# Kernel optimization log

Measured on AMD Instinct MI355X. Metric: run time of the kernel, lower is better.

## Reference

```python
import jax, jax.numpy as jnp
import numpy as np

B, H, W, C = 2, 256, 256, 96
NH, WS, SS = 3, 8, 4
HD = C // NH
N = WS * WS              # tokens per window
NWIMG = (H // WS) * (W // WS)  # windows per image
MLP = 4 * C
EPS = 1e-5

def _np_attn_mask():
    img = np.zeros((H, W))
    sl = (slice(0, -WS), slice(-WS, -SS), slice(-SS, None))
    cnt = 0
    for a in sl:
        for b in sl:
            img[a, b] = cnt
            cnt += 1
    m = img.reshape(H // WS, WS, W // WS, WS).transpose(0, 2, 1, 3).reshape(-1, N)
    am = m[:, None, :] - m[:, :, None]
    return np.where(am != 0, -100.0, 0.0).astype(np.float32)

def _np_rel_index():
    coords = np.stack(np.meshgrid(np.arange(WS), np.arange(WS), indexing='ij'))
    cf = coords.reshape(2, -1)
    rel = (cf[:, :, None] - cf[:, None, :]).transpose(1, 2, 0).copy()
    rel[..., 0] += WS - 1
    rel[..., 1] += WS - 1
    rel[..., 0] *= 2 * WS - 1
    return rel.sum(-1)

def _np_coords_table():
    r = np.arange(-(WS - 1), WS, dtype=np.float32)
    t = np.stack(np.meshgrid(r, r, indexing='ij'), axis=-1) / (WS - 1) * 8.0
    t = np.sign(t) * np.log2(np.abs(t) + 1.0) / np.log2(8.0)
    return t.reshape(-1, 2)

ATTN_MASK = jnp.asarray(_np_attn_mask())          # [NWIMG, N, N]
REL_INDEX = jnp.asarray(_np_rel_index().reshape(-1))
COORDS_TABLE = jnp.asarray(_np_coords_table())    # [(2WS-1)^2, 2]

def setup_inputs():
    key = jax.random.key(0)
    ks = jax.random.split(key, 16)
    s = 0.02
    return {
        'hidden_states': jax.random.normal(ks[0], (B, H * W, C), jnp.float32),
        'time': jax.random.uniform(ks[1], (B,), jnp.float32),
        'q_w': jax.random.normal(ks[2], (C, C), jnp.float32) * s,
        'q_b': jnp.zeros((C,), jnp.float32),
        'k_w': jax.random.normal(ks[3], (C, C), jnp.float32) * s,
        'v_w': jax.random.normal(ks[4], (C, C), jnp.float32) * s,
        'v_b': jnp.zeros((C,), jnp.float32),
        'proj_w': jax.random.normal(ks[5], (C, C), jnp.float32) * s,
        'proj_b': jnp.zeros((C,), jnp.float32),
        'logit_scale': jnp.full((NH, 1, 1), jnp.log(10.0), jnp.float32),
        'cpb_w1': jax.random.normal(ks[6], (2, 512), jnp.float32) * s,
        'cpb_b1': jnp.zeros((512,), jnp.float32),
        'cpb_w2': jax.random.normal(ks[7], (512, NH), jnp.float32) * s,
        'lnb_ww': jax.random.normal(ks[8], (1, C), jnp.float32) * s,
        'lnb_wb': jnp.ones((C,), jnp.float32),
        'lnb_bw': jax.random.normal(ks[9], (1, C), jnp.float32) * s,
        'lnb_bb': jnp.zeros((C,), jnp.float32),
        'lna_ww': jax.random.normal(ks[10], (1, C), jnp.float32) * s,
        'lna_wb': jnp.ones((C,), jnp.float32),
        'lna_bw': jax.random.normal(ks[11], (1, C), jnp.float32) * s,
        'lna_bb': jnp.zeros((C,), jnp.float32),
        'fc1_w': jax.random.normal(ks[12], (C, MLP), jnp.float32) * s,
        'fc1_b': jnp.zeros((MLP,), jnp.float32),
        'fc2_w': jax.random.normal(ks[13], (MLP, C), jnp.float32) * s,
        'fc2_b': jnp.zeros((C,), jnp.float32),
    }

def _cln(x, time, ww, wb, bw, bb):
    # ConditionalLayerNorm: stats over channels, affine params from time via Linear(1, C)
    mean = x.mean(-1, keepdims=True)
    var = (x * x).mean(-1, keepdims=True) - mean * mean
    xn = (x - mean) / jnp.sqrt(var + EPS)
    t = time.reshape(-1, 1)
    w = (t @ ww + wb)[:, None, :]
    b = (t @ bw + bb)[:, None, :]
    return w * xn + b

def reference(hidden_states, time, q_w, q_b, k_w, v_w, v_b, proj_w, proj_b, logit_scale, cpb_w1, cpb_b1, cpb_w2, lnb_ww, lnb_wb, lnb_bw, lnb_bb, lna_ww, lna_wb, lna_bw, lna_bb, fc1_w, fc1_b, fc2_w, fc2_b):
    shortcut = hidden_states
    x = hidden_states.reshape(B, H, W, C)
    x = jnp.roll(x, (-SS, -SS), axis=(1, 2))  # cyclic shift
    # window partition -> [nW, N, C]
    xw = x.reshape(B, H // WS, WS, W // WS, WS, C).transpose(0, 1, 3, 2, 4, 5).reshape(-1, N, C)
    nW = B * NWIMG
    q = (xw @ q_w + q_b).reshape(nW, N, NH, HD).transpose(0, 2, 1, 3)
    k = (xw @ k_w).reshape(nW, N, NH, HD).transpose(0, 2, 1, 3)  # key has no bias in Swinv2
    v = (xw @ v_w + v_b).reshape(nW, N, NH, HD).transpose(0, 2, 1, 3)
    # cosine attention with clamped learnable log temperature
    qn = q / jnp.maximum(jnp.linalg.norm(q, axis=-1, keepdims=True), 1e-12)
    kn = k / jnp.maximum(jnp.linalg.norm(k, axis=-1, keepdims=True), 1e-12)
    scale = jnp.exp(jnp.minimum(logit_scale, jnp.log(100.0)))  # [NH,1,1]
    attn = jnp.einsum('whnd,whmd->whnm', qn, kn) * scale[None]
    # continuous relative position bias: MLP(2->512->NH) over log-spaced coords
    bias_table = jax.nn.relu(COORDS_TABLE @ cpb_w1 + cpb_b1) @ cpb_w2
    bias = bias_table[REL_INDEX].reshape(N, N, NH).transpose(2, 0, 1)
    attn = attn + 16.0 * jax.nn.sigmoid(bias)[None]
    # shifted-window mask
    attn = attn.reshape(B, NWIMG, NH, N, N) + ATTN_MASK[None, :, None]
    attn = jax.nn.softmax(attn.reshape(nW, NH, N, N), axis=-1)
    ctx = jnp.einsum('whnm,whmd->whnd', attn, v).transpose(0, 2, 1, 3).reshape(nW, N, C)
    ctx = ctx @ proj_w + proj_b
    # window reverse + un-shift
    xr = ctx.reshape(B, H // WS, W // WS, WS, WS, C).transpose(0, 1, 3, 2, 4, 5).reshape(B, H, W, C)
    xr = jnp.roll(xr, (SS, SS), axis=(1, 2))
    attn_out = xr.reshape(B, H * W, C)
    # post-norm residual (Swin v2 style) with conditional LN
    hs = shortcut + _cln(attn_out, time, lnb_ww, lnb_wb, lnb_bw, lnb_bb)
    inter = jax.nn.gelu(hs @ fc1_w + fc1_b, approximate=False)
    mlp_out = inter @ fc2_w + fc2_b
    return hs + _cln(mlp_out, time, lna_ww, lna_wb, lna_bw, lna_bb)
```

## Files before the change

### kernel.cpp

```cpp
#include <hip/hip_runtime.h>
#include <hip/hip_bf16.h>

typedef __bf16 bf16_t;
typedef bf16_t bf16x8 __attribute__((ext_vector_type(8)));
typedef bf16_t bf16x4 __attribute__((ext_vector_type(4)));
typedef float  f32x4  __attribute__((ext_vector_type(4)));

#define LDC 104
#define LDT 72
#define LDP 70
#define LDG 392

#define WS_WQ    0
#define WS_WK    19968
#define WS_WV    39936
#define WS_WP    59904
#define WS_FC1   79872
#define WS_FC2   159744
#define WS_BIAS  235008

__device__ __forceinline__ f32x4 mfma16(bf16x8 a, bf16x8 b, f32x4 c) {
    return __builtin_amdgcn_mfma_f32_16x16x32_bf16(a, b, c, 0, 0, 0);
}

__device__ __forceinline__ float cpbf(int v) {
    float x = (float)v * (8.0f / 7.0f);
    float l = log2f(fabsf(x) + 1.0f) * (1.0f / 3.0f);
    return x < 0.f ? -l : l;
}

__device__ __forceinline__ int regcnt(int t, int hw, int ww) {
    int r = t >> 3, c = t & 7;
    int rr = (hw == 31) ? (r < 4 ? 1 : 2) : 0;
    int cc = (ww == 31) ? (c < 4 ? 1 : 2) : 0;
    return rr * 3 + cc;
}

__global__ __launch_bounds__(512) void k0_prep(
    const float* __restrict__ qw, const float* __restrict__ kw,
    const float* __restrict__ vw, const float* __restrict__ pw,
    const float* __restrict__ fc1w, const float* __restrict__ fc2w,
    const float* __restrict__ cw1, const float* __restrict__ cb1,
    const float* __restrict__ cw2, char* __restrict__ ws)
{
    int tid = threadIdx.x;
    if (blockIdx.x == 0) {
        __shared__ float part[450 * 3];
        __shared__ float table[225 * 3];
        if (tid < 450) {
            int pos = tid >> 1, half = tid & 1;
            int ia = pos / 15, ib = pos % 15;
            float c0 = cpbf(ia - 7), c1 = cpbf(ib - 7);
            float a0 = 0.f, a1 = 0.f, a2 = 0.f;
            int j0 = half * 256;
            for (int j = j0; j < j0 + 256; ++j) {
                float h = fmaf(c0, cw1[j], fmaf(c1, cw1[512 + j], cb1[j]));
                h = fmaxf(h, 0.f);
                a0 = fmaf(h, cw2[j * 3 + 0], a0);
                a1 = fmaf(h, cw2[j * 3 + 1], a1);
                a2 = fmaf(h, cw2[j * 3 + 2], a2);
            }
            part[tid * 3 + 0] = a0; part[tid * 3 + 1] = a1; part[tid * 3 + 2] = a2;
        }
        __syncthreads();
        if (tid < 225) {
            table[tid * 3 + 0] = part[(2 * tid) * 3 + 0] + part[(2 * tid + 1) * 3 + 0];
            table[tid * 3 + 1] = part[(2 * tid) * 3 + 1] + part[(2 * tid + 1) * 3 + 1];
            table[tid * 3 + 2] = part[(2 * tid) * 3 + 2] + part[(2 * tid + 1) * 3 + 2];
        }
        __syncthreads();
        float* bias = (float*)(ws + WS_BIAS);
        for (int e = tid; e < 3 * 64 * 64; e += 512) {
            int h = e >> 12, nm = e & 4095, n = nm >> 6, m = nm & 63;
            int dr = (n >> 3) - (m >> 3) + 7, dc = (n & 7) - (m & 7) + 7;
            float t = table[(dr * 15 + dc) * 3 + h];
            bias[e] = 16.f / (1.f + __expf(-t));
        }
    } else {
        int rid = (blockIdx.x - 1) * 512 + tid;
        if (rid < 9216) {
            int which = rid / 2304, r = rid % 2304;
            int i = r / 24, o4 = r % 24;
            const float* src = which == 0 ? qw : which == 1 ? kw : which == 2 ? vw : pw;
            float4 u = *(const float4*)(src + i * 96 + 4 * o4);
            bf16_t* dst = (bf16_t*)(ws + WS_WQ + which * 19968);
            dst[(4 * o4 + 0) * LDC + i] = (bf16_t)u.x;
            dst[(4 * o4 + 1) * LDC + i] = (bf16_t)u.y;
            dst[(4 * o4 + 2) * LDC + i] = (bf16_t)u.z;
            dst[(4 * o4 + 3) * LDC + i] = (bf16_t)u.w;
        } else if (rid < 18432) {
            int r = rid - 9216;
            int i = r / 96, m4 = r % 96;
            float4 u = *(const float4*)(fc1w + i * 384 + 4 * m4);
            bf16_t* dst = (bf16_t*)(ws + WS_FC1);
            dst[(4 * m4 + 0) * LDC + i] = (bf16_t)u.x;
            dst[(4 * m4 + 1) * LDC + i] = (bf16_t)u.y;
            dst[(4 * m4 + 2) * LDC + i] = (bf16_t)u.z;
            dst[(4 * m4 + 3) * LDC + i] = (bf16_t)u.w;
        } else {
            int r = rid - 18432;
            int g = r / 24, o4 = r % 24;
            float4 u = *(const float4*)(fc2w + g * 96 + 4 * o4);
            bf16_t* dst = (bf16_t*)(ws + WS_FC2);
            dst[(4 * o4 + 0) * LDG + g] = (bf16_t)u.x;
            dst[(4 * o4 + 1) * LDG + g] = (bf16_t)u.y;
            dst[(4 * o4 + 2) * LDG + g] = (bf16_t)u.z;
            dst[(4 * o4 + 3) * LDG + g] = (bf16_t)u.w;
        }
    }
}

__global__ __launch_bounds__(256, 4) void kA_attn(
    const float* __restrict__ hidden, const float* __restrict__ tv,
    const float* __restrict__ qb, const float* __restrict__ vb,
    const float* __restrict__ pb, const float* __restrict__ lsc,
    const float* __restrict__ lnww, const float* __restrict__ lnwb,
    const float* __restrict__ lnbw, const float* __restrict__ lnbb,
    const char* __restrict__ ws, float* __restrict__ hs)
{
    __shared__ __align__(16) char sm[40704];
    bf16_t* vT   = (bf16_t*)(sm + 0);
    bf16_t* qn   = (bf16_t*)(sm + 13824);
    bf16_t* kn   = (bf16_t*)(sm + 27136);
    bf16_t* P    = (bf16_t*)(sm + 13824);
    bf16_t* ctxb = (bf16_t*)(sm + 0);

    const int tid = threadIdx.x;
    const int wv = tid >> 6, lane = tid & 63, lg = lane >> 4, lr = lane & 15;
    const int wid = blockIdx.x;
    const int bat = wid >> 10, wim = wid & 1023, hw = wim >> 5, wwi = wim & 31;

    {
        bf16x8 af[3];
        {
            int tok = 16 * wv + lr;
            int gr = ((hw << 3) + (tok >> 3) + 4) & 255;
            int gc = ((wwi << 3) + (tok & 7) + 4) & 255;
            const float* xb = hidden + (((size_t)bat << 16) + (gr << 8) + gc) * 96;
            #pragma unroll
            for (int ks = 0; ks < 3; ++ks) {
                float4 u0 = *(const float4*)(xb + 32 * ks + 8 * lg);
                float4 u1 = *(const float4*)(xb + 32 * ks + 8 * lg + 4);
                bf16x8 f;
                f[0] = (bf16_t)u0.x; f[1] = (bf16_t)u0.y; f[2] = (bf16_t)u0.z; f[3] = (bf16_t)u0.w;
                f[4] = (bf16_t)u1.x; f[5] = (bf16_t)u1.y; f[6] = (bf16_t)u1.z; f[7] = (bf16_t)u1.w;
                af[ks] = f;
            }
        }
        const bf16_t* Wq = (const bf16_t*)(ws + WS_WQ);
        const bf16_t* Wk = (const bf16_t*)(ws + WS_WK);
        const bf16_t* Wv = (const bf16_t*)(ws + WS_WV);

        #pragma unroll
        for (int h = 0; h < 3; ++h) {
            f32x4 a0 = {0.f,0.f,0.f,0.f}, a1 = {0.f,0.f,0.f,0.f};
            #pragma unroll
            for (int ks = 0; ks < 3; ++ks) {
                a0 = mfma16(af[ks], *(const bf16x8*)(Wq + (32 * h + lr) * LDC + 32 * ks + 8 * lg), a0);
                a1 = mfma16(af[ks], *(const bf16x8*)(Wq + (32 * h + 16 + lr) * LDC + 32 * ks + 8 * lg), a1);
            }
            float b0 = qb[32 * h + lr], b1 = qb[32 * h + 16 + lr];
            #pragma unroll
            for (int j = 0; j < 4; ++j) { a0[j] += b0; a1[j] += b1; }
            #pragma unroll
            for (int j = 0; j < 4; ++j) {
                float s = a0[j] * a0[j] + a1[j] * a1[j];
                s += __shfl_xor(s, 1); s += __shfl_xor(s, 2); s += __shfl_xor(s, 4); s += __shfl_xor(s, 8);
                float inv = 1.f / fmaxf(sqrtf(s), 1e-12f);
                int row = 16 * wv + 4 * lg + j;
                qn[row * LDC + 32 * h + lr]      = (bf16_t)(a0[j] * inv);
                qn[row * LDC + 32 * h + 16 + lr] = (bf16_t)(a1[j] * inv);
            }
        }
        #pragma unroll
        for (int h = 0; h < 3; ++h) {
            f32x4 a0 = {0.f,0.f,0.f,0.f}, a1 = {0.f,0.f,0.f,0.f};
            #pragma unroll
            for (int ks = 0; ks < 3; ++ks) {
                a0 = mfma16(af[ks], *(const bf16x8*)(Wk + (32 * h + lr) * LDC + 32 * ks + 8 * lg), a0);
                a1 = mfma16(af[ks], *(const bf16x8*)(Wk + (32 * h + 16 + lr) * LDC + 32 * ks + 8 * lg), a1);
            }
            #pragma unroll
            for (int j = 0; j < 4; ++j) {
                float s = a0[j] * a0[j] + a1[j] * a1[j];
                s += __shfl_xor(s, 1); s += __shfl_xor(s, 2); s += __shfl_xor(s, 4); s += __shfl_xor(s, 8);
                float inv = 1.f / fmaxf(sqrtf(s), 1e-12f);
                int row = 16 * wv + 4 * lg + j;
                kn[row * LDC + 32 * h + lr]      = (bf16_t)(a0[j] * inv);
                kn[row * LDC + 32 * h + 16 + lr] = (bf16_t)(a1[j] * inv);
            }
        }
        #pragma unroll
        for (int nt = 0; nt < 6; ++nt) {
            f32x4 a = {0.f,0.f,0.f,0.f};
            #pragma unroll
            for (int ks = 0; ks < 3; ++ks)
                a = mfma16(af[ks], *(const bf16x8*)(Wv + (16 * nt + lr) * LDC + 32 * ks + 8 * lg), a);
            float bv_ = vb[16 * nt + lr];
            bf16x4 pk;
            #pragma unroll
            for (int j = 0; j < 4; ++j) pk[j] = (bf16_t)(a[j] + bv_);
            *(bf16x4*)(vT + (16 * nt + lr) * LDT + 16 * wv + 4 * lg) = pk;
        }
    }
    __syncthreads();

    {
        f32x4 s[3][4];
        #pragma unroll
        for (int h = 0; h < 3; ++h) {
            bf16x8 aq = *(const bf16x8*)(qn + (16 * wv + lr) * LDC + 32 * h + 8 * lg);
            bf16x8 bk[4];
            #pragma unroll
            for (int f = 0; f < 4; ++f)
                bk[f] = *(const bf16x8*)(kn + (16 * f + lr) * LDC + 32 * h + 8 * lg);
            #pragma unroll
            for (int f = 0; f < 4; ++f) {
                f32x4 z = {0.f,0.f,0.f,0.f};
                s[h][f] = mfma16(aq, bk[f], z);
            }
        }
        __syncthreads();

        float ls[3];
        #pragma unroll
        for (int h = 0; h < 3; ++h) ls[h] = __expf(fminf(lsc[h], 4.6051702f));
        const float* biasT = (const float*)(ws + WS_BIAS);
        int cntm[4], cnti[4];
        #pragma unroll
        for (int f = 0; f < 4; ++f) cntm[f] = regcnt(16 * f + lr, hw, wwi);
        #pragma unroll
        for (int j = 0; j < 4; ++j) cnti[j] = regcnt(16 * wv + 4 * lg + j, hw, wwi);
        #pragma unroll
        for (int h = 0; h < 3; ++h) {
            #pragma unroll
            for (int f = 0; f < 4; ++f)
                #pragma unroll
                for (int j = 0; j < 4; ++j) {
                    float b = biasT[(h << 12) + (16 * wv + 4 * lg + j) * 64 + 16 * f + lr];
                    float mk = (cnti[j] != cntm[f]) ? -100.f : 0.f;
                    s[h][f][j] = fmaf(s[h][f][j], ls[h], b + mk);
                }
            #pragma unroll
            for (int j = 0; j < 4; ++j) {
                float mx = fmaxf(fmaxf(s[h][0][j], s[h][1][j]), fmaxf(s[h][2][j], s[h][3][j]));
                mx = fmaxf(mx, __shfl_xor(mx, 1)); mx = fmaxf(mx, __shfl_xor(mx, 2));
                mx = fmaxf(mx, __shfl_xor(mx, 4)); mx = fmaxf(mx, __shfl_xor(mx, 8));
                float sum = 0.f;
                #pragma unroll
                for (int f = 0; f < 4; ++f) { float e = __expf(s[h][f][j] - mx); s[h][f][j] = e; sum += e; }
                sum += __shfl_xor(sum, 1); sum += __shfl_xor(sum, 2); sum += __shfl_xor(sum, 4); sum += __shfl_xor(sum, 8);
                float inv = 1.f / sum;
                int row = 16 * wv + 4 * lg + j;
                #pragma unroll
                for (int f = 0; f < 4; ++f)
                    P[h * 64 * LDP + row * LDP + 16 * f + lr] = (bf16_t)(s[h][f][j] * inv);
            }
        }
    }
    __syncthreads();

    {
        f32x4 ctx[6];
        #pragma unroll
        for (int t = 0; t < 6; ++t) { f32x4 z = {0.f,0.f,0.f,0.f}; ctx[t] = z; }
        #pragma unroll
        for (int h = 0; h < 3; ++h) {
            bf16x8 ap[2], bv2[2][2];
            #pragma unroll
            for (int ks = 0; ks < 2; ++ks) {
                ap[ks] = *(const bf16x8*)(P + h * 64 * LDP + (16 * wv + lr) * LDP + 32 * ks + 8 * lg);
                #pragma unroll
                for (int dt = 0; dt < 2; ++dt)
                    bv2[dt][ks] = *(const bf16x8*)(vT + (32 * h + 16 * dt + lr) * LDT + 32 * ks + 8 * lg);
            }
            #pragma unroll
            for (int ks = 0; ks < 2; ++ks)
                #pragma unroll
                for (int dt = 0; dt < 2; ++dt)
                    ctx[2 * h + dt] = mfma16(ap[ks], bv2[dt][ks], ctx[2 * h + dt]);
        }
        __syncthreads();
        #pragma unroll
        for (int t = 0; t < 6; ++t)
            #pragma unroll
            for (int j = 0; j < 4; ++j)
                ctxb[(16 * wv + 4 * lg + j) * LDC + 16 * t + lr] = (bf16_t)ctx[t][j];
    }
    __syncthreads();

    {
        const bf16_t* Wp = (const bf16_t*)(ws + WS_WP);
        bf16x8 af[3];
        #pragma unroll
        for (int ks = 0; ks < 3; ++ks) af[ks] = *(const bf16x8*)(ctxb + (16 * wv + lr) * LDC + 32 * ks + 8 * lg);
        f32x4 acc[6];
        #pragma unroll
        for (int nt = 0; nt < 6; ++nt) {
            f32x4 a = {0.f,0.f,0.f,0.f};
            #pragma unroll
            for (int ks = 0; ks < 3; ++ks)
                a = mfma16(af[ks], *(const bf16x8*)(Wp + (16 * nt + lr) * LDC + 32 * ks + 8 * lg), a);
            float bp = pb[16 * nt + lr];
            #pragma unroll
            for (int j = 0; j < 4; ++j) a[j] += bp;
            acc[nt] = a;
        }
        float tb = tv[bat];
        #pragma unroll
        for (int j = 0; j < 4; ++j) {
            float smn = 0.f, sq = 0.f;
            #pragma unroll
            for (int t = 0; t < 6; ++t) { float v = acc[t][j]; smn += v; sq = fmaf(v, v, sq); }
            smn += __shfl_xor(smn, 1); smn += __shfl_xor(smn, 2); smn += __shfl_xor(smn, 4); smn += __shfl_xor(smn, 8);
            sq  += __shfl_xor(sq, 1);  sq  += __shfl_xor(sq, 2);  sq  += __shfl_xor(sq, 4);  sq  += __shfl_xor(sq, 8);
            float mean = smn * (1.f / 96.f);
            float var  = sq * (1.f / 96.f) - mean * mean;
            float rstd = rsqrtf(var + 1e-5f);
            int trow = 16 * wv + 4 * lg + j;
            int gr = ((hw << 3) + (trow >> 3) + 4) & 255;
            int gc = ((wwi << 3) + (trow & 7) + 4) & 255;
            size_t gbase = (((size_t)bat << 16) + (gr << 8) + gc) * 96;
            #pragma unroll
            for (int t = 0; t < 6; ++t) {
                int col = 16 * t + lr;
                float w = fmaf(tb, lnww[col], lnwb[col]);
                float b = fmaf(tb, lnbw[col], lnbb[col]);
                float xn = (acc[t][j] - mean) * rstd;
                hs[gbase + col] = hidden[gbase + col] + fmaf(w, xn, b);
            }
        }
    }
}

__global__ __launch_bounds__(256, 3) void kB_mlp(
    const float* __restrict__ tv, const float* __restrict__ fc1b,
    const float* __restrict__ fc2b,
    const float* __restrict__ lnww, const float* __restrict__ lnwb,
    const float* __restrict__ lnbw, const float* __restrict__ lnbb,
    const char* __restrict__ ws, float* __restrict__ io)
{
    __shared__ __align__(16) bf16_t gbuf[64 * LDG];

    const int tid = threadIdx.x;
    const int wv = tid >> 6, lane = tid & 63, lg = lane >> 4, lr = lane & 15;
    const size_t t0 = (size_t)blockIdx.x * 64;

    bf16x8 hf[3];
    #pragma unroll
    for (int ks = 0; ks < 3; ++ks) {
        const float* p = io + (t0 + 16 * wv + lr) * 96 + 32 * ks + 8 * lg;
        float4 u0 = *(const float4*)p;
        float4 u1 = *(const float4*)(p + 4);
        bf16x8 f;
        f[0] = (bf16_t)u0.x; f[1] = (bf16_t)u0.y; f[2] = (bf16_t)u0.z; f[3] = (bf16_t)u0.w;
        f[4] = (bf16_t)u1.x; f[5] = (bf16_t)u1.y; f[6] = (bf16_t)u1.z; f[7] = (bf16_t)u1.w;
        hf[ks] = f;
    }

    const bf16_t* w1 = (const bf16_t*)(ws + WS_FC1);
    const bf16_t* w2 = (const bf16_t*)(ws + WS_FC2);

    #pragma unroll 6
    for (int nt = 0; nt < 24; ++nt) {
        f32x4 a = {0.f,0.f,0.f,0.f};
        #pragma unroll
        for (int ks = 0; ks < 3; ++ks)
            a = mfma16(hf[ks], *(const bf16x8*)(w1 + (16 * nt + lr) * LDC + 32 * ks + 8 * lg), a);
        float bb = fc1b[16 * nt + lr];
        #pragma unroll
        for (int j = 0; j < 4; ++j) {
            float x = a[j] + bb;
            float u = 0.7978845608f * fmaf(0.044715f * x, x * x, x);
            float t = __expf(2.f * u);
            float g = x - x * __builtin_amdgcn_rcpf(t + 1.f);
            gbuf[(16 * wv + 4 * lg + j) * LDG + 16 * nt + lr] = (bf16_t)g;
        }
    }
    __syncthreads();

    f32x4 mlp[6];
    #pragma unroll
    for (int t = 0; t < 6; ++t) { f32x4 z = {0.f,0.f,0.f,0.f}; mlp[t] = z; }
    #pragma unroll
    for (int kk = 0; kk < 12; ++kk) {
        bf16x8 gf = *(const bf16x8*)(gbuf + (16 * wv + lr) * LDG + 32 * kk + 8 * lg);
        #pragma unroll
        for (int nt = 0; nt < 6; ++nt)
            mlp[nt] = mfma16(gf, *(const bf16x8*)(w2 + (16 * nt + lr) * LDG + 32 * kk + 8 * lg), mlp[nt]);
    }

    float tb = tv[t0 >> 16];
    #pragma unroll
    for (int nt = 0; nt < 6; ++nt) {
        float bb = fc2b[16 * nt + lr];
        #pragma unroll
        for (int j = 0; j < 4; ++j) mlp[nt][j] += bb;
    }
    #pragma unroll
    for (int j = 0; j < 4; ++j) {
        float smn = 0.f, sq = 0.f;
        #pragma unroll
        for (int t = 0; t < 6; ++t) { float v = mlp[t][j]; smn += v; sq = fmaf(v, v, sq); }
        smn += __shfl_xor(smn, 1); smn += __shfl_xor(smn, 2); smn += __shfl_xor(smn, 4); smn += __shfl_xor(smn, 8);
        sq  += __shfl_xor(sq, 1);  sq  += __shfl_xor(sq, 2);  sq  += __shfl_xor(sq, 4);  sq  += __shfl_xor(sq, 8);
        float mean = smn * (1.f / 96.f);
        float var  = sq * (1.f / 96.f) - mean * mean;
        float rstd = rsqrtf(var + 1e-5f);
        size_t row = t0 + 16 * wv + 4 * lg + j;
        #pragma unroll
        for (int t = 0; t < 6; ++t) {
            int col = 16 * t + lr;
            float w = fmaf(tb, lnww[col], lnwb[col]);
            float b = fmaf(tb, lnbw[col], lnbb[col]);
            float xn = (mlp[t][j] - mean) * rstd;
            io[row * 96 + col] = io[row * 96 + col] + fmaf(w, xn, b);
        }
    }
}

extern "C" void kernel_launch(void* const* d_in, const int* in_sizes, int n_in,
                              void* d_out, int out_size, void* d_ws, size_t ws_size,
                              hipStream_t stream)
{
    const float* hidden = (const float*)d_in[0];
    const float* tv     = (const float*)d_in[1];
    const float* q_w    = (const float*)d_in[2];
    const float* q_b    = (const float*)d_in[3];
    const float* k_w    = (const float*)d_in[4];
    const float* v_w    = (const float*)d_in[5];
    const float* v_b    = (const float*)d_in[6];
    const float* p_w    = (const float*)d_in[7];
    const float* p_b    = (const float*)d_in[8];
    const float* lsc    = (const float*)d_in[9];
    const float* cw1    = (const float*)d_in[10];
    const float* cb1    = (const float*)d_in[11];
    const float* cw2    = (const float*)d_in[12];
    const float* lnb_ww = (const float*)d_in[13];
    const float* lnb_wb = (const float*)d_in[14];
    const float* lnb_bw = (const float*)d_in[15];
    const float* lnb_bb = (const float*)d_in[16];
    const float* lna_ww = (const float*)d_in[17];
    const float* lna_wb = (const float*)d_in[18];
    const float* lna_bw = (const float*)d_in[19];
    const float* lna_bb = (const float*)d_in[20];
    const float* fc1_w  = (const float*)d_in[21];
    const float* fc1_b  = (const float*)d_in[22];
    const float* fc2_w  = (const float*)d_in[23];
    const float* fc2_b  = (const float*)d_in[24];
    char* ws = (char*)d_ws;
    float* out = (float*)d_out;

    k0_prep<<<dim3(55), dim3(512), 0, stream>>>(q_w, k_w, v_w, p_w, fc1_w, fc2_w, cw1, cb1, cw2, ws);
    kA_attn<<<dim3(2048), dim3(256), 0, stream>>>(hidden, tv, q_b, v_b, p_b, lsc,
                                                  lnb_ww, lnb_wb, lnb_bw, lnb_bb, ws, out);
    kB_mlp<<<dim3(2048), dim3(256), 0, stream>>>(tv, fc1_b, fc2_b,
                                                 lna_ww, lna_wb, lna_bw, lna_bb, ws, out);
}
```

Baseline: 332.1 us.

## Parallelize CPB table prep and batch weight/bias loads ahead of MFMA chains

```diff
diff --git a/kernel.cpp b/kernel.cpp
--- a/kernel.cpp
+++ b/kernel.cpp
@@ -18,6 +18,7 @@
 #define WS_FC1   79872
 #define WS_FC2   159744
 #define WS_BIAS  235008
+#define WS_TBL   284160
 
 __device__ __forceinline__ f32x4 mfma16(bf16x8 a, bf16x8 b, f32x4 c) {
     return __builtin_amdgcn_mfma_f32_16x16x32_bf16(a, b, c, 0, 0, 0);
@@ -36,48 +37,46 @@
     return rr * 3 + cc;
 }
 
-__global__ __launch_bounds__(512) void k0_prep(
+__global__ __launch_bounds__(256) void k0a_cpb(
+    const float* __restrict__ cw1, const float* __restrict__ cb1,
+    const float* __restrict__ cw2, char* __restrict__ ws)
+{
+    const int wv = threadIdx.x >> 6, lane = threadIdx.x & 63;
+    const int e = blockIdx.x * 4 + wv;
+    if (e >= 225) return;
+    int ia = e / 15, ib = e % 15;
+    float c0 = cpbf(ia - 7), c1 = cpbf(ib - 7);
+    float a0 = 0.f, a1 = 0.f, a2 = 0.f;
+    #pragma unroll
+    for (int c = 0; c < 8; ++c) {
+        int j = c * 64 + lane;
+        float h = fmaf(c0, cw1[j], fmaf(c1, cw1[512 + j], cb1[j]));
+        h = fmaxf(h, 0.f);
+        a0 = fmaf(h, cw2[j * 3 + 0], a0);
+        a1 = fmaf(h, cw2[j * 3 + 1], a1);
+        a2 = fmaf(h, cw2[j * 3 + 2], a2);
+    }
+    #pragma unroll
+    for (int m = 1; m < 64; m <<= 1) {
+        a0 += __shfl_xor(a0, m);
+        a1 += __shfl_xor(a1, m);
+        a2 += __shfl_xor(a2, m);
+    }
+    if (lane == 0) {
+        float* tbl = (float*)(ws + WS_TBL);
+        tbl[e * 3 + 0] = a0; tbl[e * 3 + 1] = a1; tbl[e * 3 + 2] = a2;
+    }
+}
+
+__global__ __launch_bounds__(512) void k0w_prep(
     const float* __restrict__ qw, const float* __restrict__ kw,
     const float* __restrict__ vw, const float* __restrict__ pw,
     const float* __restrict__ fc1w, const float* __restrict__ fc2w,
-    const float* __restrict__ cw1, const float* __restrict__ cb1,
-    const float* __restrict__ cw2, char* __restrict__ ws)
+    char* __restrict__ ws)
 {
     int tid = threadIdx.x;
-    if (blockIdx.x == 0) {
-        __shared__ float part[450 * 3];
-        __shared__ float table[225 * 3];
-        if (tid < 450) {
-            int pos = tid >> 1, half = tid & 1;
-            int ia = pos / 15, ib = pos % 15;
-            float c0 = cpbf(ia - 7), c1 = cpbf(ib - 7);
-            float a0 = 0.f, a1 = 0.f, a2 = 0.f;
-            int j0 = half * 256;
-            for (int j = j0; j < j0 + 256; ++j) {
-                float h = fmaf(c0, cw1[j], fmaf(c1, cw1[512 + j], cb1[j]));
-                h = fmaxf(h, 0.f);
-                a0 = fmaf(h, cw2[j * 3 + 0], a0);
-                a1 = fmaf(h, cw2[j * 3 + 1], a1);
-                a2 = fmaf(h, cw2[j * 3 + 2], a2);
-            }
-            part[tid * 3 + 0] = a0; part[tid * 3 + 1] = a1; part[tid * 3 + 2] = a2;
-        }
-        __syncthreads();
-        if (tid < 225) {
-            table[tid * 3 + 0] = part[(2 * tid) * 3 + 0] + part[(2 * tid + 1) * 3 + 0];
-            table[tid * 3 + 1] = part[(2 * tid) * 3 + 1] + part[(2 * tid + 1) * 3 + 1];
-            table[tid * 3 + 2] = part[(2 * tid) * 3 + 2] + part[(2 * tid + 1) * 3 + 2];
-        }
-        __syncthreads();
-        float* bias = (float*)(ws + WS_BIAS);
-        for (int e = tid; e < 3 * 64 * 64; e += 512) {
-            int h = e >> 12, nm = e & 4095, n = nm >> 6, m = nm & 63;
-            int dr = (n >> 3) - (m >> 3) + 7, dc = (n & 7) - (m & 7) + 7;
-            float t = table[(dr * 15 + dc) * 3 + h];
-            bias[e] = 16.f / (1.f + __expf(-t));
-        }
-    } else {
-        int rid = (blockIdx.x - 1) * 512 + tid;
+    if (blockIdx.x < 54) {
+        int rid = blockIdx.x * 512 + tid;
         if (rid < 9216) {
             int which = rid / 2304, r = rid % 2304;
             int i = r / 24, o4 = r % 24;
@@ -107,10 +106,20 @@
             dst[(4 * o4 + 2) * LDG + g] = (bf16_t)u.z;
             dst[(4 * o4 + 3) * LDG + g] = (bf16_t)u.w;
         }
-    }
-}
-
-__global__ __launch_bounds__(256, 4) void kA_attn(
+    } else {
+        int e = (blockIdx.x - 54) * 512 + tid;
+        if (e < 12288) {
+            const float* tbl = (const float*)(ws + WS_TBL);
+            float* bias = (float*)(ws + WS_BIAS);
+            int h = e >> 12, nm = e & 4095, n = nm >> 6, m = nm & 63;
+            int dr = (n >> 3) - (m >> 3) + 7, dc = (n & 7) - (m & 7) + 7;
+            float t = tbl[(dr * 15 + dc) * 3 + h];
+            bias[e] = 16.f / (1.f + __expf(-t));
+        }
+    }
+}
+
+__global__ __launch_bounds__(256, 3) void kA_attn(
     const float* __restrict__ hidden, const float* __restrict__ tv,
     const float* __restrict__ qb, const float* __restrict__ vb,
     const float* __restrict__ pb, const float* __restrict__ lsc,
@@ -151,61 +160,96 @@
         const bf16_t* Wk = (const bf16_t*)(ws + WS_WK);
         const bf16_t* Wv = (const bf16_t*)(ws + WS_WV);
 
-        #pragma unroll
-        for (int h = 0; h < 3; ++h) {
-            f32x4 a0 = {0.f,0.f,0.f,0.f}, a1 = {0.f,0.f,0.f,0.f};
-            #pragma unroll
-            for (int ks = 0; ks < 3; ++ks) {
-                a0 = mfma16(af[ks], *(const bf16x8*)(Wq + (32 * h + lr) * LDC + 32 * ks + 8 * lg), a0);
-                a1 = mfma16(af[ks], *(const bf16x8*)(Wq + (32 * h + 16 + lr) * LDC + 32 * ks + 8 * lg), a1);
-            }
-            float b0 = qb[32 * h + lr], b1 = qb[32 * h + 16 + lr];
-            #pragma unroll
-            for (int j = 0; j < 4; ++j) { a0[j] += b0; a1[j] += b1; }
-            #pragma unroll
-            for (int j = 0; j < 4; ++j) {
-                float s = a0[j] * a0[j] + a1[j] * a1[j];
-                s += __shfl_xor(s, 1); s += __shfl_xor(s, 2); s += __shfl_xor(s, 4); s += __shfl_xor(s, 8);
-                float inv = 1.f / fmaxf(sqrtf(s), 1e-12f);
-                int row = 16 * wv + 4 * lg + j;
-                qn[row * LDC + 32 * h + lr]      = (bf16_t)(a0[j] * inv);
-                qn[row * LDC + 32 * h + 16 + lr] = (bf16_t)(a1[j] * inv);
-            }
-        }
-        #pragma unroll
-        for (int h = 0; h < 3; ++h) {
-            f32x4 a0 = {0.f,0.f,0.f,0.f}, a1 = {0.f,0.f,0.f,0.f};
-            #pragma unroll
-            for (int ks = 0; ks < 3; ++ks) {
-                a0 = mfma16(af[ks], *(const bf16x8*)(Wk + (32 * h + lr) * LDC + 32 * ks + 8 * lg), a0);
-                a1 = mfma16(af[ks], *(const bf16x8*)(Wk + (32 * h + 16 + lr) * LDC + 32 * ks + 8 * lg), a1);
-            }
-            #pragma unroll
-            for (int j = 0; j < 4; ++j) {
-                float s = a0[j] * a0[j] + a1[j] * a1[j];
-                s += __shfl_xor(s, 1); s += __shfl_xor(s, 2); s += __shfl_xor(s, 4); s += __shfl_xor(s, 8);
-                float inv = 1.f / fmaxf(sqrtf(s), 1e-12f);
-                int row = 16 * wv + 4 * lg + j;
-                kn[row * LDC + 32 * h + lr]      = (bf16_t)(a0[j] * inv);
-                kn[row * LDC + 32 * h + 16 + lr] = (bf16_t)(a1[j] * inv);
-            }
-        }
-        #pragma unroll
-        for (int nt = 0; nt < 6; ++nt) {
-            f32x4 a = {0.f,0.f,0.f,0.f};
-            #pragma unroll
-            for (int ks = 0; ks < 3; ++ks)
-                a = mfma16(af[ks], *(const bf16x8*)(Wv + (16 * nt + lr) * LDC + 32 * ks + 8 * lg), a);
-            float bv_ = vb[16 * nt + lr];
-            bf16x4 pk;
-            #pragma unroll
-            for (int j = 0; j < 4; ++j) pk[j] = (bf16_t)(a[j] + bv_);
-            *(bf16x4*)(vT + (16 * nt + lr) * LDT + 16 * wv + 4 * lg) = pk;
+        {
+            bf16x8 wf[6][3];
+            #pragma unroll
+            for (int n = 0; n < 6; ++n)
+                #pragma unroll
+                for (int ks = 0; ks < 3; ++ks)
+                    wf[n][ks] = *(const bf16x8*)(Wq + (16 * n + lr) * LDC + 32 * ks + 8 * lg);
+            f32x4 acc[6];
+            #pragma unroll
+            for (int n = 0; n < 6; ++n) {
+                f32x4 a = {0.f,0.f,0.f,0.f};
+                #pragma unroll
+                for (int ks = 0; ks < 3; ++ks) a = mfma16(af[ks], wf[n][ks], a);
+                float bq = qb[16 * n + lr];
+                #pragma unroll
+                for (int j = 0; j < 4; ++j) a[j] += bq;
+                acc[n] = a;
+            }
+            #pragma unroll
+            for (int h = 0; h < 3; ++h)
+                #pragma unroll
+                for (int j = 0; j < 4; ++j) {
+                    float s = acc[2*h][j] * acc[2*h][j] + acc[2*h+1][j] * acc[2*h+1][j];
+                    s += __shfl_xor(s, 1); s += __shfl_xor(s, 2); s += __shfl_xor(s, 4); s += __shfl_xor(s, 8);
+                    float inv = 1.f / fmaxf(sqrtf(s), 1e-12f);
+                    int row = 16 * wv + 4 * lg + j;
+                    qn[row * LDC + 32 * h + lr]      = (bf16_t)(acc[2*h][j] * inv);
+                    qn[row * LDC + 32 * h + 16 + lr] = (bf16_t)(acc[2*h+1][j] * inv);
+                }
+        }
+        {
+            bf16x8 wf[6][3];
+            #pragma unroll
+            for (int n = 0; n < 6; ++n)
+                #pragma unroll
+                for (int ks = 0; ks < 3; ++ks)
+                    wf[n][ks] = *(const bf16x8*)(Wk + (16 * n + lr) * LDC + 32 * ks + 8 * lg);
+            f32x4 acc[6];
+            #pragma unroll
+            for (int n = 0; n < 6; ++n) {
+                f32x4 a = {0.f,0.f,0.f,0.f};
+                #pragma unroll
+                for (int ks = 0; ks < 3; ++ks) a = mfma16(af[ks], wf[n][ks], a);
+                acc[n] = a;
+            }
+            #pragma unroll
+            for (int h = 0; h < 3; ++h)
+                #pragma unroll
+                for (int j = 0; j < 4; ++j) {
+                    float s = acc[2*h][j] * acc[2*h][j] + acc[2*h+1][j] * acc[2*h+1][j];
+                    s += __shfl_xor(s, 1); s += __shfl_xor(s, 2); s += __shfl_xor(s, 4); s += __shfl_xor(s, 8);
+                    float inv = 1.f / fmaxf(sqrtf(s), 1e-12f);
+                    int row = 16 * wv + 4 * lg + j;
+                    kn[row * LDC + 32 * h + lr]      = (bf16_t)(acc[2*h][j] * inv);
+                    kn[row * LDC + 32 * h + 16 + lr] = (bf16_t)(acc[2*h+1][j] * inv);
+                }
+        }
+        {
+            bf16x8 wf[6][3];
+            #pragma unroll
+            for (int n = 0; n < 6; ++n)
+                #pragma unroll
+                for (int ks = 0; ks < 3; ++ks)
+                    wf[n][ks] = *(const bf16x8*)(Wv + (16 * n + lr) * LDC + 32 * ks + 8 * lg);
+            #pragma unroll
+            for (int n = 0; n < 6; ++n) {
+                f32x4 a = {0.f,0.f,0.f,0.f};
+                #pragma unroll
+                for (int ks = 0; ks < 3; ++ks) a = mfma16(af[ks], wf[n][ks], a);
+                float bv_ = vb[16 * n + lr];
+                bf16x4 pk;
+                #pragma unroll
+                for (int j = 0; j < 4; ++j) pk[j] = (bf16_t)(a[j] + bv_);
+                *(bf16x4*)(vT + (16 * n + lr) * LDT + 16 * wv + 4 * lg) = pk;
+            }
         }
     }
     __syncthreads();
 
     {
+        float br[3][4][4];
+        const float* biasT = (const float*)(ws + WS_BIAS);
+        #pragma unroll
+        for (int h = 0; h < 3; ++h)
+            #pragma unroll
+            for (int f = 0; f < 4; ++f)
+                #pragma unroll
+                for (int j = 0; j < 4; ++j)
+                    br[h][f][j] = biasT[(h << 12) + (16 * wv + 4 * lg + j) * 64 + 16 * f + lr];
+
         f32x4 s[3][4];
         #pragma unroll
         for (int h = 0; h < 3; ++h) {
@@ -225,7 +269,6 @@
         float ls[3];
         #pragma unroll
         for (int h = 0; h < 3; ++h) ls[h] = __expf(fminf(lsc[h], 4.6051702f));
-        const float* biasT = (const float*)(ws + WS_BIAS);
         int cntm[4], cnti[4];
         #pragma unroll
         for (int f = 0; f < 4; ++f) cntm[f] = regcnt(16 * f + lr, hw, wwi);
@@ -237,9 +280,8 @@
             for (int f = 0; f < 4; ++f)
                 #pragma unroll
                 for (int j = 0; j < 4; ++j) {
-                    float b = biasT[(h << 12) + (16 * wv + 4 * lg + j) * 64 + 16 * f + lr];
                     float mk = (cnti[j] != cntm[f]) ? -100.f : 0.f;
-                    s[h][f][j] = fmaf(s[h][f][j], ls[h], b + mk);
+                    s[h][f][j] = fmaf(s[h][f][j], ls[h], br[h][f][j] + mk);
                 }
             #pragma unroll
             for (int j = 0; j < 4; ++j) {
@@ -264,22 +306,23 @@
         f32x4 ctx[6];
         #pragma unroll
         for (int t = 0; t < 6; ++t) { f32x4 z = {0.f,0.f,0.f,0.f}; ctx[t] = z; }
-        #pragma unroll
-        for (int h = 0; h < 3; ++h) {
-            bf16x8 ap[2], bv2[2][2];
+        bf16x8 ap[3][2], bv2[3][2][2];
+        #pragma unroll
+        for (int h = 0; h < 3; ++h)
             #pragma unroll
             for (int ks = 0; ks < 2; ++ks) {
-                ap[ks] = *(const bf16x8*)(P + h * 64 * LDP + (16 * wv + lr) * LDP + 32 * ks + 8 * lg);
+                ap[h][ks] = *(const bf16x8*)(P + h * 64 * LDP + (16 * wv + lr) * LDP + 32 * ks + 8 * lg);
                 #pragma unroll
                 for (int dt = 0; dt < 2; ++dt)
-                    bv2[dt][ks] = *(const bf16x8*)(vT + (32 * h + 16 * dt + lr) * LDT + 32 * ks + 8 * lg);
-            }
+                    bv2[h][dt][ks] = *(const bf16x8*)(vT + (32 * h + 16 * dt + lr) * LDT + 32 * ks + 8 * lg);
+            }
+        #pragma unroll
+        for (int h = 0; h < 3; ++h)
             #pragma unroll
             for (int ks = 0; ks < 2; ++ks)
                 #pragma unroll
                 for (int dt = 0; dt < 2; ++dt)
-                    ctx[2 * h + dt] = mfma16(ap[ks], bv2[dt][ks], ctx[2 * h + dt]);
-        }
+                    ctx[2 * h + dt] = mfma16(ap[h][ks], bv2[h][dt][ks], ctx[2 * h + dt]);
         __syncthreads();
         #pragma unroll
         for (int t = 0; t < 6; ++t)
@@ -291,22 +334,34 @@
 
     {
         const bf16_t* Wp = (const bf16_t*)(ws + WS_WP);
+        bf16x8 wf[6][3];
+        #pragma unroll
+        for (int n = 0; n < 6; ++n)
+            #pragma unroll
+            for (int ks = 0; ks < 3; ++ks)
+                wf[n][ks] = *(const bf16x8*)(Wp + (16 * n + lr) * LDC + 32 * ks + 8 * lg);
         bf16x8 af[3];
         #pragma unroll
         for (int ks = 0; ks < 3; ++ks) af[ks] = *(const bf16x8*)(ctxb + (16 * wv + lr) * LDC + 32 * ks + 8 * lg);
         f32x4 acc[6];
         #pragma unroll
-        for (int nt = 0; nt < 6; ++nt) {
+        for (int n = 0; n < 6; ++n) {
             f32x4 a = {0.f,0.f,0.f,0.f};
             #pragma unroll
-            for (int ks = 0; ks < 3; ++ks)
-                a = mfma16(af[ks], *(const bf16x8*)(Wp + (16 * nt + lr) * LDC + 32 * ks + 8 * lg), a);
-            float bp = pb[16 * nt + lr];
+            for (int ks = 0; ks < 3; ++ks) a = mfma16(af[ks], wf[n][ks], a);
+            float bp = pb[16 * n + lr];
             #pragma unroll
             for (int j = 0; j < 4; ++j) a[j] += bp;
-            acc[nt] = a;
+            acc[n] = a;
         }
         float tb = tv[bat];
+        float wco[6], bco[6];
+        #pragma unroll
+        for (int t = 0; t < 6; ++t) {
+            int col = 16 * t + lr;
+            wco[t] = fmaf(tb, lnww[col], lnwb[col]);
+            bco[t] = fmaf(tb, lnbw[col], lnbb[col]);
+        }
         #pragma unroll
         for (int j = 0; j < 4; ++j) {
             float smn = 0.f, sq = 0.f;
@@ -321,13 +376,13 @@
             int gr = ((hw << 3) + (trow >> 3) + 4) & 255;
             int gc = ((wwi << 3) + (trow & 7) + 4) & 255;
             size_t gbase = (((size_t)bat << 16) + (gr << 8) + gc) * 96;
+            float hid[6];
+            #pragma unroll
+            for (int t = 0; t < 6; ++t) hid[t] = hidden[gbase + 16 * t + lr];
             #pragma unroll
             for (int t = 0; t < 6; ++t) {
-                int col = 16 * t + lr;
-                float w = fmaf(tb, lnww[col], lnwb[col]);
-                float b = fmaf(tb, lnbw[col], lnbb[col]);
                 float xn = (acc[t][j] - mean) * rstd;
-                hs[gbase + col] = hidden[gbase + col] + fmaf(w, xn, b);
+                hs[gbase + 16 * t + lr] = hid[t] + fmaf(wco[t], xn, bco[t]);
             }
         }
     }
@@ -361,20 +416,29 @@
     const bf16_t* w1 = (const bf16_t*)(ws + WS_FC1);
     const bf16_t* w2 = (const bf16_t*)(ws + WS_FC2);
 
-    #pragma unroll 6
-    for (int nt = 0; nt < 24; ++nt) {
-        f32x4 a = {0.f,0.f,0.f,0.f};
-        #pragma unroll
-        for (int ks = 0; ks < 3; ++ks)
-            a = mfma16(hf[ks], *(const bf16x8*)(w1 + (16 * nt + lr) * LDC + 32 * ks + 8 * lg), a);
-        float bb = fc1b[16 * nt + lr];
-        #pragma unroll
-        for (int j = 0; j < 4; ++j) {
-            float x = a[j] + bb;
-            float u = 0.7978845608f * fmaf(0.044715f * x, x * x, x);
-            float t = __expf(2.f * u);
-            float g = x - x * __builtin_amdgcn_rcpf(t + 1.f);
-            gbuf[(16 * wv + 4 * lg + j) * LDG + 16 * nt + lr] = (bf16_t)g;
+    #pragma unroll
+    for (int g = 0; g < 4; ++g) {
+        bf16x8 wf[6][3];
+        #pragma unroll
+        for (int n = 0; n < 6; ++n)
+            #pragma unroll
+            for (int ks = 0; ks < 3; ++ks)
+                wf[n][ks] = *(const bf16x8*)(w1 + (16 * (6 * g + n) + lr) * LDC + 32 * ks + 8 * lg);
+        #pragma unroll
+        for (int n = 0; n < 6; ++n) {
+            int nt = 6 * g + n;
+            f32x4 a = {0.f,0.f,0.f,0.f};
+            #pragma unroll
+            for (int ks = 0; ks < 3; ++ks) a = mfma16(hf[ks], wf[n][ks], a);
+            float bb = fc1b[16 * nt + lr];
+            #pragma unroll
+            for (int j = 0; j < 4; ++j) {
+                float x = a[j] + bb;
+                float u = 0.7978845608f * fmaf(0.044715f * x, x * x, x);
+                float t = __expf(2.f * u);
+                float g2 = x - x * __builtin_amdgcn_rcpf(t + 1.f);
+                gbuf[(16 * wv + 4 * lg + j) * LDG + 16 * nt + lr] = (bf16_t)g2;
+            }
         }
     }
     __syncthreads();
@@ -383,19 +447,31 @@
     #pragma unroll
     for (int t = 0; t < 6; ++t) { f32x4 z = {0.f,0.f,0.f,0.f}; mlp[t] = z; }
     #pragma unroll
-    for (int kk = 0; kk < 12; ++kk) {
-        bf16x8 gf = *(const bf16x8*)(gbuf + (16 * wv + lr) * LDG + 32 * kk + 8 * lg);
-        #pragma unroll
-        for (int nt = 0; nt < 6; ++nt)
-            mlp[nt] = mfma16(gf, *(const bf16x8*)(w2 + (16 * nt + lr) * LDG + 32 * kk + 8 * lg), mlp[nt]);
+    for (int g = 0; g < 6; ++g) {
+        bf16x8 gf[2], wf2[2][6];
+        #pragma unroll
+        for (int u = 0; u < 2; ++u) {
+            int kk = 2 * g + u;
+            gf[u] = *(const bf16x8*)(gbuf + (16 * wv + lr) * LDG + 32 * kk + 8 * lg);
+            #pragma unroll
+            for (int n = 0; n < 6; ++n)
+                wf2[u][n] = *(const bf16x8*)(w2 + (16 * n + lr) * LDG + 32 * kk + 8 * lg);
+        }
+        #pragma unroll
+        for (int u = 0; u < 2; ++u)
+            #pragma unroll
+            for (int n = 0; n < 6; ++n)
+                mlp[n] = mfma16(gf[u], wf2[u][n], mlp[n]);
     }
 
     float tb = tv[t0 >> 16];
-    #pragma unroll
-    for (int nt = 0; nt < 6; ++nt) {
-        float bb = fc2b[16 * nt + lr];
-        #pragma unroll
-        for (int j = 0; j < 4; ++j) mlp[nt][j] += bb;
+    float wco[6], bco[6];
+    #pragma unroll
+    for (int t = 0; t < 6; ++t) {
+        int col = 16 * t + lr;
+        wco[t] = fmaf(tb, lnww[col], lnwb[col]);
+        bco[t] = fmaf(tb, lnbw[col], lnbb[col]);
+        mlp[t][0] += fc2b[col]; mlp[t][1] += fc2b[col]; mlp[t][2] += fc2b[col]; mlp[t][3] += fc2b[col];
     }
     #pragma unroll
     for (int j = 0; j < 4; ++j) {
@@ -408,13 +484,13 @@
         float var  = sq * (1.f / 96.f) - mean * mean;
         float rstd = rsqrtf(var + 1e-5f);
         size_t row = t0 + 16 * wv + 4 * lg + j;
+        float hid[6];
+        #pragma unroll
+        for (int t = 0; t < 6; ++t) hid[t] = io[row * 96 + 16 * t + lr];
         #pragma unroll
         for (int t = 0; t < 6; ++t) {
-            int col = 16 * t + lr;
-            float w = fmaf(tb, lnww[col], lnwb[col]);
-            float b = fmaf(tb, lnbw[col], lnbb[col]);
             float xn = (mlp[t][j] - mean) * rstd;
-            io[row * 96 + col] = io[row * 96 + col] + fmaf(w, xn, b);
+            io[row * 96 + 16 * t + lr] = hid[t] + fmaf(wco[t], xn, bco[t]);
         }
     }
 }
@@ -451,7 +527,8 @@
     char* ws = (char*)d_ws;
     float* out = (float*)d_out;
 
-    k0_prep<<<dim3(55), dim3(512), 0, stream>>>(q_w, k_w, v_w, p_w, fc1_w, fc2_w, cw1, cb1, cw2, ws);
+    k0a_cpb<<<dim3(57), dim3(256), 0, stream>>>(cw1, cb1, cw2, ws);
+    k0w_prep<<<dim3(78), dim3(512), 0, stream>>>(q_w, k_w, v_w, p_w, fc1_w, fc2_w, ws);
     kA_attn<<<dim3(2048), dim3(256), 0, stream>>>(hidden, tv, q_b, v_b, p_b, lsc,
                                                   lnb_ww, lnb_wb, lnb_bw, lnb_bb, ws, out);
     kB_mlp<<<dim3(2048), dim3(256), 0, stream>>>(tv, fc1_b, fc2_b,
```

New measurement: 284.5 us. 14.3% less time.
